# Performance work log

Hardware: AMD Instinct MI355X
Metric: run time of the kernel (lower is better)

## Reference

```python
import jax, jax.numpy as jnp
import numpy as np

SAMPLE_RATE = 44100
NUM_FILTERS = 3
FREQ_LO, FREQ_HI = 100.0, 3000.0
Q_LO, Q_HI = 1.0, 5.0
GAIN_LO, GAIN_HI = -24.0, 24.0


def _center_freqs():
    # power_ratio(i/N, f_lo, f_hi) = f_lo * (f_hi/f_lo)**(i/N)
    return [FREQ_LO * (FREQ_HI / FREQ_LO) ** (i / NUM_FILTERS) for i in range(NUM_FILTERS)]


def setup_inputs() -> dict:
    key = jax.random.key(0)
    k1, k2, k3 = jax.random.split(key, 3)
    audio = jax.random.normal(k1, (32, 441000), dtype=jnp.float32)  # [B, T]
    # Q sampled like power_ratio(u, q_lo, q_hi) = q_lo*(q_hi/q_lo)**u
    u = jax.random.uniform(k2, (NUM_FILTERS,), dtype=jnp.float32)
    qs = Q_LO * (Q_HI / Q_LO) ** u
    gains = jax.random.uniform(k3, (NUM_FILTERS,), dtype=jnp.float32,
                               minval=GAIN_LO, maxval=GAIN_HI)
    return {"audio": audio, "qs": qs, "gains": gains}


def _biquad(x, b0, b1, b2, a1, a2):
    """Direct-form-I biquad over time axis. x: [B, T]; coeffs normalized by a0."""
    B = x.shape[0]
    z = jnp.zeros((B,), x.dtype)

    def step(carry, xn):
        x1, x2, y1, y2 = carry
        yn = b0 * xn + b1 * x1 + b2 * x2 - a1 * y1 - a2 * y2
        return (xn, x1, yn, y1), yn

    _, y = jax.lax.scan(step, (z, z, z, z), x.T)  # scan over T
    return y.T


def _peaking_eq(audio, center_freq, gain, Q):
    # torchaudio.functional.equalizer_biquad coefficients
    w0 = 2.0 * jnp.pi * center_freq / SAMPLE_RATE
    alpha = jnp.sin(w0) / (2.0 * Q)
    A = jnp.exp(gain / 40.0 * jnp.log(10.0))  # 10**(gain/40)
    b0 = 1.0 + alpha * A
    b1 = -2.0 * jnp.cos(w0)
    b2 = 1.0 - alpha * A
    a0 = 1.0 + alpha / A
    a1 = -2.0 * jnp.cos(w0)
    a2 = 1.0 - alpha / A
    return _biquad(audio, b0 / a0, b1 / a0, b2 / a0, a1 / a0, a2 / a0)


def reference(audio, qs, gains):
    cfs = _center_freqs()
    for i in range(NUM_FILTERS):
        audio = _peaking_eq(audio, cfs[i], gains[i], qs[i])
    return audio
```

## Files before the change

kernel.cpp:

```cpp
#include <hip/hip_runtime.h>
#include <math.h>

#define SR      44100.0
#define T_LEN   441000
#define B_ROWS  32
#define CHUNK   32
#define NCH     13782
#define WPR     216
#define NWAVE   (B_ROWS * WPR)
#define NBLK    (NWAVE / 4)
#define NSEG    8
#define SEGCH   1724
#define ROUNDS  10

#define WS_T    0
#define WS_E    2048
#define WS_F    1576960

typedef __attribute__((address_space(1))) const void gconst_t;
typedef __attribute__((address_space(3))) void lds_t;
#define GL2LDS(gp, lp) __builtin_amdgcn_global_load_lds((gconst_t*)(gp), (lds_t*)(lp), 16, 0, 0)


#define COMPUTE_COEFS_TO_LDS(scoef, qs, gains) do { \
    if (threadIdx.x < 3) { \
      int f = threadIdx.x; \
      double cfq = 100.0 * exp(log(30.0) * (double)f / 3.0); \
      double w0 = 2.0 * M_PI * cfq / SR; \
      double alpha = sin(w0) / (2.0 * (double)qs[f]); \
      double Ag = exp((double)gains[f] * (2.302585092994045684 / 40.0)); \
      double a0 = 1.0 + alpha / Ag; \
      scoef[f*5+0] = (float)((1.0 + alpha * Ag) / a0); \
      scoef[f*5+1] = (float)((-2.0 * cos(w0)) / a0); \
      scoef[f*5+2] = (float)((1.0 - alpha * Ag) / a0); \
      scoef[f*5+3] = (float)((-2.0 * cos(w0)) / a0); \
      scoef[f*5+4] = (float)((1.0 - alpha / Ag) / a0); \
    } \
  } while (0)

#define LOAD_COEFS(cf) \
  const float b00=cf[0],b10=cf[1],b20=cf[2],a10=cf[3],a20=cf[4]; \
  const float b01=cf[5],b11=cf[6],b21=cf[7],a11=cf[8],a21=cf[9]; \
  const float b02=cf[10],b12=cf[11],b22=cf[12],a12=cf[13],a22=cf[14];

#define CASCADE_STEP(xx) do { \
    float y1 = fmaf(b00, (xx), s11); \
    s11 = fmaf(-a10, y1, fmaf(b10, (xx), s21)); \
    s21 = fmaf(-a20, y1, b20 * (xx)); \
    float y2 = fmaf(b01, y1, s12); \
    s12 = fmaf(-a11, y2, fmaf(b11, y1, s22)); \
    s22 = fmaf(-a21, y2, b21 * y1); \
    y3 = fmaf(b02, y2, s13); \
    s13 = fmaf(-a12, y3, fmaf(b12, y2, s23)); \
    s23 = fmaf(-a22, y3, b22 * y2); \
  } while (0)

#define MV6(dst, M, v, add) do { \
    _Pragma("unroll") \
    for (int _i = 0; _i < 6; _i++) { \
      float _s = (add)[_i]; \
      _Pragma("unroll") \
      for (int _k = 0; _k < 6; _k++) _s = fmaf((M)[_i*6+_k], (v)[_k], _s); \
      (dst)[_i] = _s; \
    } \
  } while (0)


__global__ __launch_bounds__(256) void kA_states(const float* __restrict__ x,
                                                 const float* __restrict__ qs,
                                                 const float* __restrict__ gains,
                                                 float* __restrict__ ws) {
  __shared__ float lds[4 * 2048];
  __shared__ float scoef[16];
  int wib = threadIdx.x >> 6, lane = threadIdx.x & 63;
  int gw = blockIdx.x * 4 + wib;
  int row = gw / WPR, wci = gw % WPR;
  long rowbase = (long)row * T_LEN;
  int s0 = wci << 11;
  int span4 = (min(2048, T_LEN - s0)) >> 2;
  const float4* xp = (const float4*)(x + rowbase + s0);
  float* slab = lds + (wib << 11);
  if (span4 == 512) {
    #pragma unroll
    for (int i = 0; i < 8; i++) {
      int s = (i << 6) + lane;
      int g = (s & ~7) | ((s & 7) ^ ((s >> 3) & 7));
      GL2LDS(xp + g, slab + (i << 8));
    }
  } else {
    #pragma unroll
    for (int i = 0; i < 8; i++) {
      int s = (i << 6) + lane;
      int g = (s & ~7) | ((s & 7) ^ ((s >> 3) & 7));
      if (g < span4) GL2LDS(xp + g, slab + (i << 8));
    }
  }
  COMPUTE_COEFS_TO_LDS(scoef, qs, gains);
  __syncthreads();
  int ci = (wci << 6) + lane;
  if (ci < NCH) {
    LOAD_COEFS(scoef);
    int rem = min(CHUNK, T_LEN - (ci << 5));
    int n4 = rem >> 2;
    const float* rowp = slab + (lane << 5);
    int xr = lane & 7;
    float s11=0,s21=0,s12=0,s22=0,s13=0,s23=0, y3;
    if (n4 == 8) {
      #pragma unroll
      for (int j4 = 0; j4 < 8; j4++) {
        float4 v = *(const float4*)(rowp + ((j4 ^ xr) << 2));
        CASCADE_STEP(v.x); CASCADE_STEP(v.y); CASCADE_STEP(v.z); CASCADE_STEP(v.w);
      }
    } else {
      for (int j4 = 0; j4 < n4; j4++) {
        float4 v = *(const float4*)(rowp + ((j4 ^ xr) << 2));
        CASCADE_STEP(v.x); CASCADE_STEP(v.y); CASCADE_STEP(v.z); CASCADE_STEP(v.w);
      }
    }
    (void)y3;
    float2* F = (float2*)(ws + WS_F + ((long)row * NCH + ci) * 6);
    F[0] = make_float2(s11, s21); F[1] = make_float2(s12, s22); F[2] = make_float2(s13, s23);
  }
}


__device__ __forceinline__ void mm6d(const double* X, const double* Y, double* Z, int t) {
  if (t < 36) {
    int i = t / 6, j = t % 6;
    double s = 0.0;
    #pragma unroll
    for (int k = 0; k < 6; k++) s += X[i*6+k] * Y[k*6+j];
    Z[t] = s;
  }
}

template<bool WANT_G>
__device__ __forceinline__ void scan_setup(const float* qs, const float* gains, int t,
                                           double* Da, double* Db, double* Dc, double* Dd,
                                           float* sW, float (*sV)[36], float* sG) {
  __shared__ double dco[3][5];
  if (t < 3) {
    int f = t;
    double cfq = 100.0 * exp(log(30.0) * (double)f / 3.0);
    double w0 = 2.0 * M_PI * cfq / SR;
    double alpha = sin(w0) / (2.0 * (double)qs[f]);
    double Ag = exp((double)gains[f] * (2.302585092994045684 / 40.0));
    double a0 = 1.0 + alpha / Ag;
    dco[f][0] = (1.0 + alpha * Ag) / a0;
    dco[f][1] = (-2.0 * cos(w0)) / a0;
    dco[f][2] = (1.0 - alpha * Ag) / a0;
    dco[f][3] = (-2.0 * cos(w0)) / a0;
    dco[f][4] = (1.0 - alpha / Ag) / a0;
  }
  __syncthreads();
  if (t == 0) {
    double u[7] = {0,0,0,0,0,0,1};
    for (int f = 0; f < 3; f++) {
      double b0=dco[f][0], b1=dco[f][1], b2=dco[f][2], a1=dco[f][3], a2=dco[f][4];
      double yv[7], s1p[7], s2p[7];
      for (int i = 0; i < 7; i++) {
        yv[i]  = b0 * u[i] + ((i == 2*f)   ? 1.0 : 0.0);
        s1p[i] = b1 * u[i] + ((i == 2*f+1) ? 1.0 : 0.0) - a1 * yv[i];
        s2p[i] = b2 * u[i] - a2 * yv[i];
      }
      for (int i = 0; i < 6; i++) { Da[(2*f)*6+i] = s1p[i]; Da[(2*f+1)*6+i] = s2p[i]; }
      for (int i = 0; i < 7; i++) u[i] = yv[i];
    }
  }
  if (WANT_G && t < 36) Dc[t] = (t % 7 == 0) ? 1.0 : 0.0;
  __syncthreads();
  mm6d(Da, Da, Db, t); __syncthreads();
  mm6d(Db, Db, Da, t); __syncthreads();
  mm6d(Da, Da, Db, t); __syncthreads();
  mm6d(Db, Db, Da, t); __syncthreads();
  mm6d(Da, Da, Db, t); __syncthreads();
  if (t < 36) sW[t] = (float)Db[t];
  mm6d(Db, Db, Da, t); __syncthreads();
  double* cur = Da; double* oth = Db;
  double* Gc = Dc; double* Gd = Dd;
  #pragma unroll
  for (int k = 0; k < ROUNDS; k++) {
    if (t < 36) sV[k][t] = (float)cur[t];
    if (WANT_G && ((SEGCH >> (k + 1)) & 1)) {
      __syncthreads();
      mm6d(Gc, cur, Gd, t); __syncthreads();
      double* tm = Gc; Gc = Gd; Gd = tm;
    }
    if (k < ROUNDS - 1) {
      __syncthreads();
      mm6d(cur, cur, oth, t); __syncthreads();
      double* tm = cur; cur = oth; oth = tm;
    }
  }
  if (WANT_G && t < 36) sG[t] = (float)Gc[t];
  __syncthreads();
}


__global__ __launch_bounds__(1024) void kB1_scan(const float* __restrict__ qs,
                                                 const float* __restrict__ gains,
                                                 float* __restrict__ ws) {
  int seg = blockIdx.x & 7, row = blockIdx.x >> 3, t = threadIdx.x;
  __shared__ double Da[36], Db[36], Dc[36], Dd[36];
  __shared__ float sW[36], sV[ROUNDS][36];
  __shared__ float bufA[1024][7], bufB[1024][7];
  scan_setup<false>(qs, gains, t, Da, Db, Dc, Dd, sW, sV, nullptr);

  int segstart = seg * SEGCH;
  int nch = min(SEGCH, NCH - segstart);
  int nact = nch >> 1;
  const float* F = ws + WS_F + ((long)row * NCH + segstart) * 6;
  float v[6] = {0,0,0,0,0,0};
  if (t < nact) {
    const float4* Fp = (const float4*)(F + 12 * t);
    float4 l0 = Fp[0], l1 = Fp[1], l2 = Fp[2];
    float f0[6] = {l0.x, l0.y, l0.z, l0.w, l1.x, l1.y};
    float f1[6] = {l1.z, l1.w, l2.x, l2.y, l2.z, l2.w};
    MV6(v, sW, f0, f1);
  }
  #pragma unroll
  for (int i = 0; i < 6; i++) bufA[t][i] = v[i];
  __syncthreads();
  float (*src)[7] = bufA, (*dst)[7] = bufB;
  for (int k = 0; k < ROUNDS; k++) {
    int d = 1 << k;
    float nv[6];
    if (t >= d) {
      MV6(nv, sV[k], src[t-d], src[t]);
    } else {
      #pragma unroll
      for (int i = 0; i < 6; i++) nv[i] = src[t][i];
    }
    #pragma unroll
    for (int i = 0; i < 6; i++) dst[t][i] = nv[i];
    __syncthreads();
    float (*tm)[7] = src; src = dst; dst = tm;
  }
  float* Ep = ws + WS_E + ((long)blockIdx.x * 1024 + t) * 6;
  if (t > 0) {
    #pragma unroll
    for (int i = 0; i < 6; i++) Ep[i] = src[t-1][i];
  } else {
    #pragma unroll
    for (int i = 0; i < 6; i++) Ep[i] = 0.0f;
  }
  if (t == nact - 1) {
    float* Tp = ws + WS_T + (long)blockIdx.x * 6;
    #pragma unroll
    for (int i = 0; i < 6; i++) Tp[i] = src[t][i];
  }
}


__global__ __launch_bounds__(1024) void kB2_inject(const float* __restrict__ qs,
                                                   const float* __restrict__ gains,
                                                   float* __restrict__ ws) {
  int seg = blockIdx.x & 7, row = blockIdx.x >> 3, t = threadIdx.x;
  __shared__ double Da[36], Db[36], Dc[36], Dd[36];
  __shared__ float sW[36], sV[ROUNDS][36], sG[36];
  __shared__ float sT[8][6], sO[6];
  scan_setup<true>(qs, gains, t, Da, Db, Dc, Dd, sW, sV, sG);
  if (t < 48) sT[t/6][t%6] = ws[WS_T + ((long)(row*8) + t/6) * 6 + t%6];
  __syncthreads();
  if (t == 0) {
    float o[6] = {0,0,0,0,0,0};
    for (int s2 = 0; s2 < seg; s2++) {
      float no[6];
      MV6(no, sG, o, sT[s2]);
      #pragma unroll
      for (int i = 0; i < 6; i++) o[i] = no[i];
    }
    #pragma unroll
    for (int i = 0; i < 6; i++) sO[i] = o[i];
  }
  __syncthreads();
  int segstart = seg * SEGCH;
  int nch = min(SEGCH, NCH - segstart);
  int nact = nch >> 1;
  if (t < nact) {
    float e[6];
    #pragma unroll
    for (int i = 0; i < 6; i++) e[i] = sO[i];
    for (int k = 0; k < ROUNDS; k++) {
      if ((t >> k) & 1) {
        float z[6] = {0,0,0,0,0,0}, ne[6];
        MV6(ne, sV[k], e, z);
        #pragma unroll
        for (int i = 0; i < 6; i++) e[i] = ne[i];
      }
    }
    const float* Er = ws + WS_E + ((long)blockIdx.x * 1024 + t) * 6;
    #pragma unroll
    for (int i = 0; i < 6; i++) e[i] += Er[i];
    float4* Fp = (float4*)(ws + WS_F + ((long)row * NCH + segstart) * 6 + 12 * t);
    float4 l0 = Fp[0], l1 = Fp[1], l2 = Fp[2];
    float f0[6] = {l0.x, l0.y, l0.z, l0.w, l1.x, l1.y};
    float e1[6];
    MV6(e1, sW, e, f0);
    (void)l2;
    Fp[0] = make_float4(e[0], e[1], e[2], e[3]);
    Fp[1] = make_float4(e[4], e[5], e1[0], e1[1]);
    Fp[2] = make_float4(e1[2], e1[3], e1[4], e1[5]);
  }
}


__global__ __launch_bounds__(256) void kC_emit(const float* __restrict__ x,
                                               const float* __restrict__ qs,
                                               const float* __restrict__ gains,
                                               float* __restrict__ y,
                                               const float* __restrict__ ws) {
  __shared__ float lds[4 * 2048];
  __shared__ float scoef[16];
  int wib = threadIdx.x >> 6, lane = threadIdx.x & 63;
  int gw = blockIdx.x * 4 + wib;
  int row = gw / WPR, wci = gw % WPR;
  long rowbase = (long)row * T_LEN;
  int s0 = wci << 11;
  int span4 = (min(2048, T_LEN - s0)) >> 2;
  const float4* xp = (const float4*)(x + rowbase + s0);
  float* slab = lds + (wib << 11);
  if (span4 == 512) {
    #pragma unroll
    for (int i = 0; i < 8; i++) {
      int s = (i << 6) + lane;
      int g = (s & ~7) | ((s & 7) ^ ((s >> 3) & 7));
      GL2LDS(xp + g, slab + (i << 8));
    }
  } else {
    #pragma unroll
    for (int i = 0; i < 8; i++) {
      int s = (i << 6) + lane;
      int g = (s & ~7) | ((s & 7) ^ ((s >> 3) & 7));
      if (g < span4) GL2LDS(xp + g, slab + (i << 8));
    }
  }
  COMPUTE_COEFS_TO_LDS(scoef, qs, gains);
  int ci = (wci << 6) + lane;
  float e0=0,e1=0,e2=0,e3=0,e4=0,e5=0;
  if (ci < NCH) {
    const float2* E = (const float2*)(ws + WS_F + ((long)row * NCH + ci) * 6);
    float2 a = E[0], b = E[1], c = E[2];
    e0=a.x; e1=a.y; e2=b.x; e3=b.y; e4=c.x; e5=c.y;
  }
  __syncthreads();
  if (ci < NCH) {
    LOAD_COEFS(scoef);
    float s11=e0, s21=e1, s12=e2, s22=e3, s13=e4, s23=e5;
    int rem = min(CHUNK, T_LEN - (ci << 5));
    int n4 = rem >> 2;
    float* rowp = slab + (lane << 5);
    int xr = lane & 7;
    float y3;
    if (n4 == 8) {
      #pragma unroll
      for (int j4 = 0; j4 < 8; j4++) {
        float* p = rowp + ((j4 ^ xr) << 2);
        float4 v = *(const float4*)p;
        float4 o;
        CASCADE_STEP(v.x); o.x = y3;
        CASCADE_STEP(v.y); o.y = y3;
        CASCADE_STEP(v.z); o.z = y3;
        CASCADE_STEP(v.w); o.w = y3;
        *(float4*)p = o;
      }
    } else {
      for (int j4 = 0; j4 < n4; j4++) {
        float* p = rowp + ((j4 ^ xr) << 2);
        float4 v = *(const float4*)p;
        float4 o;
        CASCADE_STEP(v.x); o.x = y3;
        CASCADE_STEP(v.y); o.y = y3;
        CASCADE_STEP(v.z); o.z = y3;
        CASCADE_STEP(v.w); o.w = y3;
        *(float4*)p = o;
      }
    }
  }
  __syncthreads();
  float4* yp = (float4*)(y + rowbase + s0);
  if (span4 == 512) {
    #pragma unroll
    for (int i = 0; i < 8; i++) {
      int g = (i << 6) + lane;
      int s = (g & ~7) | ((g & 7) ^ ((g >> 3) & 7));
      yp[g] = *(const float4*)(slab + (s << 2));
    }
  } else {
    #pragma unroll
    for (int i = 0; i < 8; i++) {
      int g = (i << 6) + lane;
      int s = (g & ~7) | ((g & 7) ^ ((g >> 3) & 7));
      if (g < span4) yp[g] = *(const float4*)(slab + (s << 2));
    }
  }
}

extern "C" void kernel_launch(void* const* d_in, const int* in_sizes, int n_in,
                              void* d_out, int out_size, void* d_ws, size_t ws_size,
                              hipStream_t stream) {
  const float* audio = (const float*)d_in[0];
  const float* qs    = (const float*)d_in[1];
  const float* gains = (const float*)d_in[2];
  float* out = (float*)d_out;
  float* ws  = (float*)d_ws;

  hipLaunchKernelGGL(kA_states, dim3(NBLK), dim3(256), 0, stream, audio, qs, gains, ws);
  hipLaunchKernelGGL(kB1_scan, dim3(B_ROWS * NSEG), dim3(1024), 0, stream, qs, gains, ws);
  hipLaunchKernelGGL(kB2_inject, dim3(B_ROWS * NSEG), dim3(1024), 0, stream, qs, gains, ws);
  hipLaunchKernelGGL(kC_emit, dim3(NBLK), dim3(256), 0, stream, audio, qs, gains, out, ws);
}
```

Before: 68.58 us.

## Fuse four-kernel biquad scan into one cooperative persistent kernel with grid syncs

Replaces the chain of four launches (chunk states, segment scan, inject, emit) with a single cooperative kernel. Each thread keeps its 32 input samples in registers across grid.sync barriers, so the input is read from global memory once, and the scan is re-partitioned into 32 segments per row run by the first 1024 blocks. It also adds readfirstlane for the filter coefficients. The aim is to remove launch gaps and the second input read, at the cost of grid-wide barriers, a serial per-block segment-prefix loop, and host-side occupancy queries on every call, with the old path kept as a fallback.

```diff
diff --git a/kernel.cpp b/kernel.cpp
--- a/kernel.cpp
+++ b/kernel.cpp
@@ -1,21 +1,29 @@
 #include <hip/hip_runtime.h>
+#include <hip/hip_cooperative_groups.h>
 #include <math.h>
+
+namespace cg = cooperative_groups;
 
 #define SR      44100.0
 #define T_LEN   441000
 #define B_ROWS  32
-#define CHUNK   32
 #define NCH     13782
+#define GCH     (B_ROWS * NCH)
+#define FNB     1723
+#define NSCAN   1024
+#define FSEGW   432
+#define FROUNDS 8
+
+#define FWS_T   0
+#define FWS_F   8192
+
+#define R5SEGCH 1724
+#define R5ROUNDS 10
+#define R5WS_T  0
+#define R5WS_E  2048
+#define R5WS_F  1576960
 #define WPR     216
-#define NWAVE   (B_ROWS * WPR)
-#define NBLK    (NWAVE / 4)
-#define NSEG    8
-#define SEGCH   1724
-#define ROUNDS  10
-
-#define WS_T    0
-#define WS_E    2048
-#define WS_F    1576960
+#define R5NBLK  1728
 
 typedef __attribute__((address_space(1))) const void gconst_t;
 typedef __attribute__((address_space(3))) void lds_t;
@@ -43,6 +51,14 @@
   const float b01=cf[5],b11=cf[6],b21=cf[7],a11=cf[8],a21=cf[9]; \
   const float b02=cf[10],b12=cf[11],b22=cf[12],a12=cf[13],a22=cf[14];
 
+__device__ __forceinline__ float rfl(float v) {
+  return __int_as_float(__builtin_amdgcn_readfirstlane(__float_as_int(v)));
+}
+#define LOAD_COEFS_RFL(cf) \
+  const float b00=rfl(cf[0]),b10=rfl(cf[1]),b20=rfl(cf[2]),a10=rfl(cf[3]),a20=rfl(cf[4]); \
+  const float b01=rfl(cf[5]),b11=rfl(cf[6]),b21=rfl(cf[7]),a11=rfl(cf[8]),a21=rfl(cf[9]); \
+  const float b02=rfl(cf[10]),b12=rfl(cf[11]),b22=rfl(cf[12]),a12=rfl(cf[13]),a22=rfl(cf[14]);
+
 #define CASCADE_STEP(xx) do { \
     float y1 = fmaf(b00, (xx), s11); \
     s11 = fmaf(-a10, y1, fmaf(b10, (xx), s21)); \
@@ -64,6 +80,322 @@
       (dst)[_i] = _s; \
     } \
   } while (0)
+
+__device__ __forceinline__ void mm6d(const double* X, const double* Y, double* Z, int t) {
+  if (t < 36) {
+    int i = t / 6, j = t % 6;
+    double s = 0.0;
+    #pragma unroll
+    for (int k = 0; k < 6; k++) s += X[i*6+k] * Y[k*6+j];
+    Z[t] = s;
+  }
+}
+
+
+#define STAGE_IN(h) do { \
+    _Pragma("unroll") \
+    for (int i = 0; i < 4; i++) { \
+      int t_ = (i << 6) + lane; \
+      int c_ = t_ >> 3; \
+      int q_ = (t_ & 7) ^ (c_ & 7); \
+      int gc_ = wc0 + ((h) << 5) + c_; \
+      unsigned r_ = (unsigned)gc_ / NCH; \
+      int ci_ = gc_ - (int)r_ * NCH; \
+      long s4_ = (long)r_ * 110250 + ci_ * 8 + q_; \
+      if (gc_ < GCH && s4_ < 3528000L) GL2LDS(xp4 + s4_, slab + (t_ << 2)); \
+    } \
+  } while (0)
+
+#define READ_HALF(h) do { \
+    if ((lane >> 5) == (h) && cvalid) { \
+      const float* rowp_ = slab + ((lane & 31) << 5); \
+      int xr_ = lane & 7; \
+      _Pragma("unroll") \
+      for (int j4 = 0; j4 < 8; j4++) a[j4] = *(const float4*)(rowp_ + ((j4 ^ xr_) << 2)); \
+    } \
+  } while (0)
+
+#define OUT_HALF(h) do { \
+    if ((lane >> 5) == (h) && cvalid) { \
+      float* rowp_ = slab + ((lane & 31) << 5); \
+      int xr_ = lane & 7; \
+      _Pragma("unroll") \
+      for (int j4 = 0; j4 < 8; j4++) *(float4*)(rowp_ + ((j4 ^ xr_) << 2)) = a[j4]; \
+    } \
+  } while (0)
+
+#define OUT_STORE(h) do { \
+    _Pragma("unroll") \
+    for (int i = 0; i < 4; i++) { \
+      int t_ = (i << 6) + lane; \
+      int c_ = t_ >> 3, q_ = t_ & 7; \
+      int gs_ = (t_ & ~7) | (q_ ^ (c_ & 7)); \
+      int gc_ = wc0 + ((h) << 5) + c_; \
+      unsigned r_ = (unsigned)gc_ / NCH; \
+      int ci_ = gc_ - (int)r_ * NCH; \
+      int n4c_ = (ci_ == NCH - 1) ? 2 : 8; \
+      if (gc_ < GCH && q_ < n4c_) \
+        ((float4*)y)[(long)r_ * 110250 + ci_ * 8 + q_] = *(const float4*)(slab + (gs_ << 2)); \
+    } \
+  } while (0)
+
+__global__ __launch_bounds__(256, 7) void fused(const float* __restrict__ x,
+                                                const float* __restrict__ qs,
+                                                const float* __restrict__ gains,
+                                                float* __restrict__ y,
+                                                float* __restrict__ ws) {
+  cg::grid_group grid = cg::this_grid();
+  __shared__ __align__(16) float smem[4736];
+  const int tid = threadIdx.x;
+  const int wib = tid >> 6, lane = tid & 63;
+  float* slab  = smem + (wib << 10);
+  float* scoef = smem + 4096;
+  float* sW    = smem + 4112;
+  float* sV    = smem + 4148;
+  float* sT    = smem + 4436;
+  float* sO    = smem + 4628;
+  float* sG    = smem + 4640;
+  const int wc0 = blockIdx.x * 256 + (wib << 6);
+  const int gchunk = blockIdx.x * 256 + tid;
+  const bool cvalid = gchunk < GCH;
+  const float4* xp4 = (const float4*)x;
+  float4 a[8];
+
+  STAGE_IN(0);
+  COMPUTE_COEFS_TO_LDS(scoef, qs, gains);
+  __syncthreads();
+  READ_HALF(0);
+  __syncthreads();
+  STAGE_IN(1);
+  __syncthreads();
+  READ_HALF(1);
+  LOAD_COEFS_RFL(scoef);
+  {
+    unsigned r = (unsigned)gchunk / NCH;
+    int ci = gchunk - (int)r * NCH;
+    int n4 = (ci == NCH - 1) ? 2 : 8;
+    if (cvalid) {
+      float s11=0,s21=0,s12=0,s22=0,s13=0,s23=0, y3;
+      if (n4 == 8) {
+        #pragma unroll
+        for (int j4 = 0; j4 < 8; j4++) {
+          CASCADE_STEP(a[j4].x); CASCADE_STEP(a[j4].y);
+          CASCADE_STEP(a[j4].z); CASCADE_STEP(a[j4].w);
+        }
+      } else {
+        CASCADE_STEP(a[0].x); CASCADE_STEP(a[0].y); CASCADE_STEP(a[0].z); CASCADE_STEP(a[0].w);
+        CASCADE_STEP(a[1].x); CASCADE_STEP(a[1].y); CASCADE_STEP(a[1].z); CASCADE_STEP(a[1].w);
+      }
+      (void)y3;
+      float2* F2 = (float2*)(ws + FWS_F + (long)gchunk * 6);
+      F2[0] = make_float2(s11, s21); F2[1] = make_float2(s12, s22); F2[2] = make_float2(s13, s23);
+    }
+  }
+  grid.sync();
+
+  const bool isScan = blockIdx.x < NSCAN;
+  if (isScan) {
+    double* D = (double*)smem;
+    double* Da = D, *Db = D+36, *Dc = D+72, *Dd = D+108, *dco = D+144;
+    if (tid < 3) {
+      int f = tid;
+      double cfq = 100.0 * exp(log(30.0) * (double)f / 3.0);
+      double w0 = 2.0 * M_PI * cfq / SR;
+      double alpha = sin(w0) / (2.0 * (double)qs[f]);
+      double Ag = exp((double)gains[f] * (2.302585092994045684 / 40.0));
+      double a0 = 1.0 + alpha / Ag;
+      dco[f*5+0] = (1.0 + alpha * Ag) / a0;
+      dco[f*5+1] = (-2.0 * cos(w0)) / a0;
+      dco[f*5+2] = (1.0 - alpha * Ag) / a0;
+      dco[f*5+3] = (-2.0 * cos(w0)) / a0;
+      dco[f*5+4] = (1.0 - alpha / Ag) / a0;
+    }
+    __syncthreads();
+    if (tid == 0) {
+      double u[7] = {0,0,0,0,0,0,1};
+      for (int f = 0; f < 3; f++) {
+        double b0=dco[f*5+0], b1=dco[f*5+1], b2=dco[f*5+2], a1=dco[f*5+3], a2=dco[f*5+4];
+        double yv[7], s1p[7], s2p[7];
+        for (int i = 0; i < 7; i++) {
+          yv[i]  = b0 * u[i] + ((i == 2*f)   ? 1.0 : 0.0);
+          s1p[i] = b1 * u[i] + ((i == 2*f+1) ? 1.0 : 0.0) - a1 * yv[i];
+          s2p[i] = b2 * u[i] - a2 * yv[i];
+        }
+        for (int i = 0; i < 6; i++) { Da[(2*f)*6+i] = s1p[i]; Da[(2*f+1)*6+i] = s2p[i]; }
+        for (int i = 0; i < 7; i++) u[i] = yv[i];
+      }
+    }
+    __syncthreads();
+    mm6d(Da, Da, Db, tid); __syncthreads();
+    mm6d(Db, Db, Da, tid); __syncthreads();
+    mm6d(Da, Da, Db, tid); __syncthreads();
+    mm6d(Db, Db, Da, tid); __syncthreads();
+    mm6d(Da, Da, Db, tid); __syncthreads();
+    if (tid < 36) { sW[tid] = (float)Db[tid]; Dc[tid] = (tid % 7 == 0) ? 1.0 : 0.0; }
+    __syncthreads();
+    mm6d(Db, Db, Da, tid); __syncthreads();
+    {
+      double* cur = Da; double* oth = Db; double* Gc = Dc; double* Gd = Dd;
+      #pragma unroll
+      for (int k = 0; k < FROUNDS; k++) {
+        if (tid < 36) sV[k*36 + tid] = (float)cur[tid];
+        if ((FSEGW >> (k + 1)) & 1) {
+          __syncthreads();
+          mm6d(Gc, cur, Gd, tid); __syncthreads();
+          double* tm = Gc; Gc = Gd; Gd = tm;
+        }
+        if (k < FROUNDS - 1) {
+          __syncthreads();
+          mm6d(cur, cur, oth, tid); __syncthreads();
+          double* tm = cur; cur = oth; oth = tm;
+        }
+      }
+      if (tid < 36) sG[tid] = (float)Gc[tid];
+    }
+    __syncthreads();
+
+    int srow = blockIdx.x >> 5, seg = blockIdx.x & 31;
+    int segstart = seg * FSEGW;
+    int nact = (seg == 31) ? 195 : 216;
+    float* bufA = smem;
+    float* bufB = smem + 1792;
+    float e_rel[6], f0[6];
+    {
+      float v[6] = {0,0,0,0,0,0};
+      if (tid < nact) {
+        const float4* Fp = (const float4*)(ws + FWS_F + ((long)srow*NCH + segstart + 2*tid) * 6);
+        float4 l0 = Fp[0], l1 = Fp[1], l2 = Fp[2];
+        f0[0]=l0.x; f0[1]=l0.y; f0[2]=l0.z; f0[3]=l0.w; f0[4]=l1.x; f0[5]=l1.y;
+        float f1[6] = {l1.z, l1.w, l2.x, l2.y, l2.z, l2.w};
+        MV6(v, sW, f0, f1);
+      }
+      #pragma unroll
+      for (int i = 0; i < 6; i++) bufA[tid*7 + i] = v[i];
+      __syncthreads();
+      float* src = bufA; float* dst = bufB;
+      for (int k = 0; k < FROUNDS; k++) {
+        int d = 1 << k;
+        float nv[6];
+        if (tid >= d) { MV6(nv, sV + k*36, src + (tid-d)*7, src + tid*7); }
+        else { 
+          #pragma unroll
+          for (int i = 0; i < 6; i++) nv[i] = src[tid*7 + i];
+        }
+        #pragma unroll
+        for (int i = 0; i < 6; i++) dst[tid*7 + i] = nv[i];
+        __syncthreads();
+        float* tm = src; src = dst; dst = tm;
+      }
+      if (tid > 0) {
+        #pragma unroll
+        for (int i = 0; i < 6; i++) e_rel[i] = src[(tid-1)*7 + i];
+      } else {
+        #pragma unroll
+        for (int i = 0; i < 6; i++) e_rel[i] = 0.0f;
+      }
+      if (tid == nact - 1) {
+        #pragma unroll
+        for (int i = 0; i < 6; i++) ws[FWS_T + (long)blockIdx.x * 6 + i] = src[tid*7 + i];
+      }
+    }
+    grid.sync();
+    if (tid < 192) sT[tid] = ws[FWS_T + srow*192 + tid];
+    __syncthreads();
+    if (tid == 0) {
+      float o[6] = {0,0,0,0,0,0};
+      for (int s2 = 0; s2 < seg; s2++) {
+        float no[6];
+        MV6(no, sG, o, sT + s2*6);
+        #pragma unroll
+        for (int i = 0; i < 6; i++) o[i] = no[i];
+      }
+      #pragma unroll
+      for (int i = 0; i < 6; i++) sO[i] = o[i];
+    }
+    __syncthreads();
+    if (tid < nact) {
+      float e[6];
+      #pragma unroll
+      for (int i = 0; i < 6; i++) e[i] = sO[i];
+      float z6[6] = {0,0,0,0,0,0};
+      for (int k = 0; k < FROUNDS; k++) {
+        if ((tid >> k) & 1) {
+          float ne[6];
+          MV6(ne, sV + k*36, e, z6);
+          #pragma unroll
+          for (int i = 0; i < 6; i++) e[i] = ne[i];
+        }
+      }
+      #pragma unroll
+      for (int i = 0; i < 6; i++) e[i] += e_rel[i];
+      float e1[6];
+      MV6(e1, sW, e, f0);
+      float4* Fp = (float4*)(ws + FWS_F + ((long)srow*NCH + segstart + 2*tid) * 6);
+      Fp[0] = make_float4(e[0], e[1], e[2], e[3]);
+      Fp[1] = make_float4(e[4], e[5], e1[0], e1[1]);
+      Fp[2] = make_float4(e1[2], e1[3], e1[4], e1[5]);
+    }
+    grid.sync();
+    STAGE_IN(0);
+    __syncthreads();
+    READ_HALF(0);
+    __syncthreads();
+    STAGE_IN(1);
+    __syncthreads();
+    READ_HALF(1);
+  } else {
+    grid.sync();
+    grid.sync();
+  }
+
+  {
+    float e0=0,e1v=0,e2=0,e3=0,e4=0,e5=0;
+    if (cvalid) {
+      const float2* E = (const float2*)(ws + FWS_F + (long)gchunk * 6);
+      float2 p0 = E[0], p1 = E[1], p2 = E[2];
+      e0=p0.x; e1v=p0.y; e2=p1.x; e3=p1.y; e4=p2.x; e5=p2.y;
+    }
+    unsigned r = (unsigned)gchunk / NCH;
+    int ci = gchunk - (int)r * NCH;
+    int n4 = (ci == NCH - 1) ? 2 : 8;
+    if (cvalid) {
+      float s11=e0, s21=e1v, s12=e2, s22=e3, s13=e4, s23=e5;
+      float y3;
+      if (n4 == 8) {
+        #pragma unroll
+        for (int j4 = 0; j4 < 8; j4++) {
+          float4 v = a[j4], o;
+          CASCADE_STEP(v.x); o.x = y3;
+          CASCADE_STEP(v.y); o.y = y3;
+          CASCADE_STEP(v.z); o.z = y3;
+          CASCADE_STEP(v.w); o.w = y3;
+          a[j4] = o;
+        }
+      } else {
+        float4 v = a[0], o;
+        CASCADE_STEP(v.x); o.x = y3;
+        CASCADE_STEP(v.y); o.y = y3;
+        CASCADE_STEP(v.z); o.z = y3;
+        CASCADE_STEP(v.w); o.w = y3;
+        a[0] = o;
+        v = a[1];
+        CASCADE_STEP(v.x); o.x = y3;
+        CASCADE_STEP(v.y); o.y = y3;
+        CASCADE_STEP(v.z); o.z = y3;
+        CASCADE_STEP(v.w); o.w = y3;
+        a[1] = o;
+      }
+    }
+  }
+  __syncthreads();
+  OUT_HALF(0);
+  __syncthreads();
+  OUT_STORE(0);
+  __syncthreads();
+  OUT_HALF(1);
+  __syncthreads();
+  OUT_STORE(1);
+}
 
 
 __global__ __launch_bounds__(256) void kA_states(const float* __restrict__ x,
@@ -80,57 +412,29 @@
   int span4 = (min(2048, T_LEN - s0)) >> 2;
   const float4* xp = (const float4*)(x + rowbase + s0);
   float* slab = lds + (wib << 11);
-  if (span4 == 512) {
-    #pragma unroll
-    for (int i = 0; i < 8; i++) {
-      int s = (i << 6) + lane;
-      int g = (s & ~7) | ((s & 7) ^ ((s >> 3) & 7));
-      GL2LDS(xp + g, slab + (i << 8));
-    }
-  } else {
-    #pragma unroll
-    for (int i = 0; i < 8; i++) {
-      int s = (i << 6) + lane;
-      int g = (s & ~7) | ((s & 7) ^ ((s >> 3) & 7));
-      if (g < span4) GL2LDS(xp + g, slab + (i << 8));
-    }
+  #pragma unroll
+  for (int i = 0; i < 8; i++) {
+    int s = (i << 6) + lane;
+    int g = (s & ~7) | ((s & 7) ^ ((s >> 3) & 7));
+    if (g < span4) GL2LDS(xp + g, slab + (i << 8));
   }
   COMPUTE_COEFS_TO_LDS(scoef, qs, gains);
   __syncthreads();
   int ci = (wci << 6) + lane;
   if (ci < NCH) {
     LOAD_COEFS(scoef);
-    int rem = min(CHUNK, T_LEN - (ci << 5));
+    int rem = min(32, T_LEN - (ci << 5));
     int n4 = rem >> 2;
     const float* rowp = slab + (lane << 5);
     int xr = lane & 7;
     float s11=0,s21=0,s12=0,s22=0,s13=0,s23=0, y3;
-    if (n4 == 8) {
-      #pragma unroll
-      for (int j4 = 0; j4 < 8; j4++) {
-        float4 v = *(const float4*)(rowp + ((j4 ^ xr) << 2));
-        CASCADE_STEP(v.x); CASCADE_STEP(v.y); CASCADE_STEP(v.z); CASCADE_STEP(v.w);
-      }
-    } else {
-      for (int j4 = 0; j4 < n4; j4++) {
-        float4 v = *(const float4*)(rowp + ((j4 ^ xr) << 2));
-        CASCADE_STEP(v.x); CASCADE_STEP(v.y); CASCADE_STEP(v.z); CASCADE_STEP(v.w);
-      }
+    for (int j4 = 0; j4 < n4; j4++) {
+      float4 v = *(const float4*)(rowp + ((j4 ^ xr) << 2));
+      CASCADE_STEP(v.x); CASCADE_STEP(v.y); CASCADE_STEP(v.z); CASCADE_STEP(v.w);
     }
     (void)y3;
-    float2* F = (float2*)(ws + WS_F + ((long)row * NCH + ci) * 6);
+    float2* F = (float2*)(ws + R5WS_F + ((long)row * NCH + ci) * 6);
     F[0] = make_float2(s11, s21); F[1] = make_float2(s12, s22); F[2] = make_float2(s13, s23);
-  }
-}
-
-
-__device__ __forceinline__ void mm6d(const double* X, const double* Y, double* Z, int t) {
-  if (t < 36) {
-    int i = t / 6, j = t % 6;
-    double s = 0.0;
-    #pragma unroll
-    for (int k = 0; k < 6; k++) s += X[i*6+k] * Y[k*6+j];
-    Z[t] = s;
   }
 }
 
@@ -179,14 +483,14 @@
   double* cur = Da; double* oth = Db;
   double* Gc = Dc; double* Gd = Dd;
   #pragma unroll
-  for (int k = 0; k < ROUNDS; k++) {
+  for (int k = 0; k < R5ROUNDS; k++) {
     if (t < 36) sV[k][t] = (float)cur[t];
-    if (WANT_G && ((SEGCH >> (k + 1)) & 1)) {
+    if (WANT_G && ((R5SEGCH >> (k + 1)) & 1)) {
       __syncthreads();
       mm6d(Gc, cur, Gd, t); __syncthreads();
       double* tm = Gc; Gc = Gd; Gd = tm;
     }
-    if (k < ROUNDS - 1) {
+    if (k < R5ROUNDS - 1) {
       __syncthreads();
       mm6d(cur, cur, oth, t); __syncthreads();
       double* tm = cur; cur = oth; oth = tm;
@@ -195,21 +499,19 @@
   if (WANT_G && t < 36) sG[t] = (float)Gc[t];
   __syncthreads();
 }
-
 
 __global__ __launch_bounds__(1024) void kB1_scan(const float* __restrict__ qs,
                                                  const float* __restrict__ gains,
                                                  float* __restrict__ ws) {
   int seg = blockIdx.x & 7, row = blockIdx.x >> 3, t = threadIdx.x;
   __shared__ double Da[36], Db[36], Dc[36], Dd[36];
-  __shared__ float sW[36], sV[ROUNDS][36];
+  __shared__ float sW[36], sV[R5ROUNDS][36];
   __shared__ float bufA[1024][7], bufB[1024][7];
   scan_setup<false>(qs, gains, t, Da, Db, Dc, Dd, sW, sV, nullptr);
-
-  int segstart = seg * SEGCH;
-  int nch = min(SEGCH, NCH - segstart);
+  int segstart = seg * R5SEGCH;
+  int nch = min(R5SEGCH, NCH - segstart);
   int nact = nch >> 1;
-  const float* F = ws + WS_F + ((long)row * NCH + segstart) * 6;
+  const float* F = ws + R5WS_F + ((long)row * NCH + segstart) * 6;
   float v[6] = {0,0,0,0,0,0};
   if (t < nact) {
     const float4* Fp = (const float4*)(F + 12 * t);
@@ -222,12 +524,11 @@
   for (int i = 0; i < 6; i++) bufA[t][i] = v[i];
   __syncthreads();
   float (*src)[7] = bufA, (*dst)[7] = bufB;
-  for (int k = 0; k < ROUNDS; k++) {
+  for (int k = 0; k < R5ROUNDS; k++) {
     int d = 1 << k;
     float nv[6];
-    if (t >= d) {
-      MV6(nv, sV[k], src[t-d], src[t]);
-    } else {
+    if (t >= d) { MV6(nv, sV[k], src[t-d], src[t]); }
+    else {
       #pragma unroll
       for (int i = 0; i < 6; i++) nv[i] = src[t][i];
     }
@@ -236,7 +537,7 @@
     __syncthreads();
     float (*tm)[7] = src; src = dst; dst = tm;
   }
-  float* Ep = ws + WS_E + ((long)blockIdx.x * 1024 + t) * 6;
+  float* Ep = ws + R5WS_E + ((long)blockIdx.x * 1024 + t) * 6;
   if (t > 0) {
     #pragma unroll
     for (int i = 0; i < 6; i++) Ep[i] = src[t-1][i];
@@ -245,22 +546,21 @@
     for (int i = 0; i < 6; i++) Ep[i] = 0.0f;
   }
   if (t == nact - 1) {
-    float* Tp = ws + WS_T + (long)blockIdx.x * 6;
+    float* Tp = ws + R5WS_T + (long)blockIdx.x * 6;
     #pragma unroll
     for (int i = 0; i < 6; i++) Tp[i] = src[t][i];
   }
 }
-
 
 __global__ __launch_bounds__(1024) void kB2_inject(const float* __restrict__ qs,
                                                    const float* __restrict__ gains,
                                                    float* __restrict__ ws) {
   int seg = blockIdx.x & 7, row = blockIdx.x >> 3, t = threadIdx.x;
   __shared__ double Da[36], Db[36], Dc[36], Dd[36];
-  __shared__ float sW[36], sV[ROUNDS][36], sG[36];
+  __shared__ float sW[36], sV[R5ROUNDS][36], sG[36];
   __shared__ float sT[8][6], sO[6];
   scan_setup<true>(qs, gains, t, Da, Db, Dc, Dd, sW, sV, sG);
-  if (t < 48) sT[t/6][t%6] = ws[WS_T + ((long)(row*8) + t/6) * 6 + t%6];
+  if (t < 48) sT[t/6][t%6] = ws[R5WS_T + ((long)(row*8) + t/6) * 6 + t%6];
   __syncthreads();
   if (t == 0) {
     float o[6] = {0,0,0,0,0,0};
@@ -274,14 +574,14 @@
     for (int i = 0; i < 6; i++) sO[i] = o[i];
   }
   __syncthreads();
-  int segstart = seg * SEGCH;
-  int nch = min(SEGCH, NCH - segstart);
+  int segstart = seg * R5SEGCH;
+  int nch = min(R5SEGCH, NCH - segstart);
   int nact = nch >> 1;
   if (t < nact) {
     float e[6];
     #pragma unroll
     for (int i = 0; i < 6; i++) e[i] = sO[i];
-    for (int k = 0; k < ROUNDS; k++) {
+    for (int k = 0; k < R5ROUNDS; k++) {
       if ((t >> k) & 1) {
         float z[6] = {0,0,0,0,0,0}, ne[6];
         MV6(ne, sV[k], e, z);
@@ -289,21 +589,19 @@
         for (int i = 0; i < 6; i++) e[i] = ne[i];
       }
     }
-    const float* Er = ws + WS_E + ((long)blockIdx.x * 1024 + t) * 6;
+    const float* Er = ws + R5WS_E + ((long)blockIdx.x * 1024 + t) * 6;
     #pragma unroll
     for (int i = 0; i < 6; i++) e[i] += Er[i];
-    float4* Fp = (float4*)(ws + WS_F + ((long)row * NCH + segstart) * 6 + 12 * t);
-    float4 l0 = Fp[0], l1 = Fp[1], l2 = Fp[2];
+    float4* Fp = (float4*)(ws + R5WS_F + ((long)row * NCH + segstart) * 6 + 12 * t);
+    float4 l0 = Fp[0], l1 = Fp[1];
     float f0[6] = {l0.x, l0.y, l0.z, l0.w, l1.x, l1.y};
     float e1[6];
     MV6(e1, sW, e, f0);
-    (void)l2;
     Fp[0] = make_float4(e[0], e[1], e[2], e[3]);
     Fp[1] = make_float4(e[4], e[5], e1[0], e1[1]);
     Fp[2] = make_float4(e1[2], e1[3], e1[4], e1[5]);
   }
 }
-
 
 __global__ __launch_bounds__(256) void kC_emit(const float* __restrict__ x,
                                                const float* __restrict__ qs,
@@ -320,79 +618,47 @@
   int span4 = (min(2048, T_LEN - s0)) >> 2;
   const float4* xp = (const float4*)(x + rowbase + s0);
   float* slab = lds + (wib << 11);
-  if (span4 == 512) {
-    #pragma unroll
-    for (int i = 0; i < 8; i++) {
-      int s = (i << 6) + lane;
-      int g = (s & ~7) | ((s & 7) ^ ((s >> 3) & 7));
-      GL2LDS(xp + g, slab + (i << 8));
-    }
-  } else {
-    #pragma unroll
-    for (int i = 0; i < 8; i++) {
-      int s = (i << 6) + lane;
-      int g = (s & ~7) | ((s & 7) ^ ((s >> 3) & 7));
-      if (g < span4) GL2LDS(xp + g, slab + (i << 8));
-    }
+  #pragma unroll
+  for (int i = 0; i < 8; i++) {
+    int s = (i << 6) + lane;
+    int g = (s & ~7) | ((s & 7) ^ ((s >> 3) & 7));
+    if (g < span4) GL2LDS(xp + g, slab + (i << 8));
   }
   COMPUTE_COEFS_TO_LDS(scoef, qs, gains);
   int ci = (wci << 6) + lane;
   float e0=0,e1=0,e2=0,e3=0,e4=0,e5=0;
   if (ci < NCH) {
-    const float2* E = (const float2*)(ws + WS_F + ((long)row * NCH + ci) * 6);
-    float2 a = E[0], b = E[1], c = E[2];
-    e0=a.x; e1=a.y; e2=b.x; e3=b.y; e4=c.x; e5=c.y;
+    const float2* E = (const float2*)(ws + R5WS_F + ((long)row * NCH + ci) * 6);
+    float2 p0 = E[0], p1 = E[1], p2 = E[2];
+    e0=p0.x; e1=p0.y; e2=p1.x; e3=p1.y; e4=p2.x; e5=p2.y;
   }
   __syncthreads();
   if (ci < NCH) {
     LOAD_COEFS(scoef);
     float s11=e0, s21=e1, s12=e2, s22=e3, s13=e4, s23=e5;
-    int rem = min(CHUNK, T_LEN - (ci << 5));
+    int rem = min(32, T_LEN - (ci << 5));
     int n4 = rem >> 2;
     float* rowp = slab + (lane << 5);
     int xr = lane & 7;
     float y3;
-    if (n4 == 8) {
-      #pragma unroll
-      for (int j4 = 0; j4 < 8; j4++) {
-        float* p = rowp + ((j4 ^ xr) << 2);
-        float4 v = *(const float4*)p;
-        float4 o;
-        CASCADE_STEP(v.x); o.x = y3;
-        CASCADE_STEP(v.y); o.y = y3;
-        CASCADE_STEP(v.z); o.z = y3;
-        CASCADE_STEP(v.w); o.w = y3;
-        *(float4*)p = o;
-      }
-    } else {
-      for (int j4 = 0; j4 < n4; j4++) {
-        float* p = rowp + ((j4 ^ xr) << 2);
-        float4 v = *(const float4*)p;
-        float4 o;
-        CASCADE_STEP(v.x); o.x = y3;
-        CASCADE_STEP(v.y); o.y = y3;
-        CASCADE_STEP(v.z); o.z = y3;
-        CASCADE_STEP(v.w); o.w = y3;
-        *(float4*)p = o;
-      }
+    for (int j4 = 0; j4 < n4; j4++) {
+      float* p = rowp + ((j4 ^ xr) << 2);
+      float4 v = *(const float4*)p;
+      float4 o;
+      CASCADE_STEP(v.x); o.x = y3;
+      CASCADE_STEP(v.y); o.y = y3;
+      CASCADE_STEP(v.z); o.z = y3;
+      CASCADE_STEP(v.w); o.w = y3;
+      *(float4*)p = o;
     }
   }
   __syncthreads();
   float4* yp = (float4*)(y + rowbase + s0);
-  if (span4 == 512) {
-    #pragma unroll
-    for (int i = 0; i < 8; i++) {
-      int g = (i << 6) + lane;
-      int s = (g & ~7) | ((g & 7) ^ ((g >> 3) & 7));
-      yp[g] = *(const float4*)(slab + (s << 2));
-    }
-  } else {
-    #pragma unroll
-    for (int i = 0; i < 8; i++) {
-      int g = (i << 6) + lane;
-      int s = (g & ~7) | ((g & 7) ^ ((g >> 3) & 7));
-      if (g < span4) yp[g] = *(const float4*)(slab + (s << 2));
-    }
+  #pragma unroll
+  for (int i = 0; i < 8; i++) {
+    int g = (i << 6) + lane;
+    int s = (g & ~7) | ((g & 7) ^ ((g >> 3) & 7));
+    if (g < span4) yp[g] = *(const float4*)(lds + (wib << 11) + (s << 2));
   }
 }
 
@@ -405,8 +671,24 @@
   float* out = (float*)d_out;
   float* ws  = (float*)d_ws;
 
-  hipLaunchKernelGGL(kA_states, dim3(NBLK), dim3(256), 0, stream, audio, qs, gains, ws);
-  hipLaunchKernelGGL(kB1_scan, dim3(B_ROWS * NSEG), dim3(1024), 0, stream, qs, gains, ws);
-  hipLaunchKernelGGL(kB2_inject, dim3(B_ROWS * NSEG), dim3(1024), 0, stream, qs, gains, ws);
-  hipLaunchKernelGGL(kC_emit, dim3(NBLK), dim3(256), 0, stream, audio, qs, gains, out, ws);
-}
+  int dev = 0;
+  (void)hipGetDevice(&dev);
+  int nb = 0;
+  (void)hipOccupancyMaxActiveBlocksPerMultiprocessor(&nb, fused, 256, 0);
+  int ncu = 0;
+  (void)hipDeviceGetAttribute(&ncu, hipDeviceAttributeMultiprocessorCount, dev);
+
+  hipError_t st = hipErrorUnknown;
+  if ((long)nb * ncu >= FNB) {
+    void* kargs[] = {(void*)&audio, (void*)&qs, (void*)&gains, (void*)&out, (void*)&ws};
+    st = hipLaunchCooperativeKernel((const void*)fused, dim3(FNB), dim3(256),
+                                    kargs, 0, stream);
+  }
+  if (st != hipSuccess) {
+    (void)hipGetLastError();
+    hipLaunchKernelGGL(kA_states, dim3(R5NBLK), dim3(256), 0, stream, audio, qs, gains, ws);
+    hipLaunchKernelGGL(kB1_scan, dim3(B_ROWS * 8), dim3(1024), 0, stream, qs, gains, ws);
+    hipLaunchKernelGGL(kB2_inject, dim3(B_ROWS * 8), dim3(1024), 0, stream, qs, gains, ws);
+    hipLaunchKernelGGL(kC_emit, dim3(R5NBLK), dim3(256), 0, stream, audio, qs, gains, out, ws);
+  }
+}
```

Measured after the change: 69.67 us. Within noise of the previous version (+1.6%).

## Merge scan and inject kernels, move cross-segment carry injection into emit kernel

Applied to the files above, without the earlier changes.

Removes the separate kB2_inject kernel. The scan kernel now writes each segment's local exclusive prefix state directly into the F buffer, plus the segment totals and the power matrices to workspace. The emit kernel then computes the per-segment carry with the G matrix and propagates it to each chunk using binary powers of the transition matrix before running the cascade. This saves one kernel launch and the extra workspace round trip for E, at the cost of up to 11 6x6 matrix-vector products per thread plus a serial carry loop in emit. It also relies on block 0 writing the matrices that every block in the later kernel reads, which is safe because the writes happen in a previous launch on the same stream.

```diff
diff --git a/kernel.cpp b/kernel.cpp
--- a/kernel.cpp
+++ b/kernel.cpp
@@ -4,8 +4,8 @@
 #define SR      44100.0
 #define T_LEN   441000
 #define B_ROWS  32
-#define CHUNK   32
 #define NCH     13782
+#define GCH     (B_ROWS * NCH)
 #define WPR     216
 #define NWAVE   (B_ROWS * WPR)
 #define NBLK    (NWAVE / 4)
@@ -13,9 +13,9 @@
 #define SEGCH   1724
 #define ROUNDS  10
 
-#define WS_T    0
-#define WS_E    2048
-#define WS_F    1576960
+#define WS_MAT  0
+#define WS_T    512
+#define WS_F    4096
 
 typedef __attribute__((address_space(1))) const void gconst_t;
 typedef __attribute__((address_space(3))) void lds_t;
@@ -65,6 +65,16 @@
     } \
   } while (0)
 
+__device__ __forceinline__ void mm6d(const double* X, const double* Y, double* Z, int t) {
+  if (t < 36) {
+    int i = t / 6, j = t % 6;
+    double s = 0.0;
+    #pragma unroll
+    for (int k = 0; k < 6; k++) s += X[i*6+k] * Y[k*6+j];
+    Z[t] = s;
+  }
+}
+
 
 __global__ __launch_bounds__(256) void kA_states(const float* __restrict__ x,
                                                  const float* __restrict__ qs,
@@ -100,7 +110,7 @@
   int ci = (wci << 6) + lane;
   if (ci < NCH) {
     LOAD_COEFS(scoef);
-    int rem = min(CHUNK, T_LEN - (ci << 5));
+    int rem = min(32, T_LEN - (ci << 5));
     int n4 = rem >> 2;
     const float* rowp = slab + (lane << 5);
     int xr = lane & 7;
@@ -124,17 +134,6 @@
 }
 
 
-__device__ __forceinline__ void mm6d(const double* X, const double* Y, double* Z, int t) {
-  if (t < 36) {
-    int i = t / 6, j = t % 6;
-    double s = 0.0;
-    #pragma unroll
-    for (int k = 0; k < 6; k++) s += X[i*6+k] * Y[k*6+j];
-    Z[t] = s;
-  }
-}
-
-template<bool WANT_G>
 __device__ __forceinline__ void scan_setup(const float* qs, const float* gains, int t,
                                            double* Da, double* Db, double* Dc, double* Dd,
                                            float* sW, float (*sV)[36], float* sG) {
@@ -167,7 +166,7 @@
       for (int i = 0; i < 7; i++) u[i] = yv[i];
     }
   }
-  if (WANT_G && t < 36) Dc[t] = (t % 7 == 0) ? 1.0 : 0.0;
+  if (t < 36) Dc[t] = (t % 7 == 0) ? 1.0 : 0.0;
   __syncthreads();
   mm6d(Da, Da, Db, t); __syncthreads();
   mm6d(Db, Db, Da, t); __syncthreads();
@@ -181,7 +180,7 @@
   #pragma unroll
   for (int k = 0; k < ROUNDS; k++) {
     if (t < 36) sV[k][t] = (float)cur[t];
-    if (WANT_G && ((SEGCH >> (k + 1)) & 1)) {
+    if ((SEGCH >> (k + 1)) & 1) {
       __syncthreads();
       mm6d(Gc, cur, Gd, t); __syncthreads();
       double* tm = Gc; Gc = Gd; Gd = tm;
@@ -192,29 +191,35 @@
       double* tm = cur; cur = oth; oth = tm;
     }
   }
-  if (WANT_G && t < 36) sG[t] = (float)Gc[t];
-  __syncthreads();
-}
-
-
-__global__ __launch_bounds__(1024) void kB1_scan(const float* __restrict__ qs,
-                                                 const float* __restrict__ gains,
-                                                 float* __restrict__ ws) {
+  if (t < 36) sG[t] = (float)Gc[t];
+  __syncthreads();
+}
+
+
+__global__ __launch_bounds__(1024) void kB_scan(const float* __restrict__ qs,
+                                                const float* __restrict__ gains,
+                                                float* __restrict__ ws) {
   int seg = blockIdx.x & 7, row = blockIdx.x >> 3, t = threadIdx.x;
   __shared__ double Da[36], Db[36], Dc[36], Dd[36];
-  __shared__ float sW[36], sV[ROUNDS][36];
+  __shared__ float sW[36], sV[ROUNDS][36], sG[36];
   __shared__ float bufA[1024][7], bufB[1024][7];
-  scan_setup<false>(qs, gains, t, Da, Db, Dc, Dd, sW, sV, nullptr);
-
+  scan_setup(qs, gains, t, Da, Db, Dc, Dd, sW, sV, sG);
+  if (blockIdx.x == 0 && t < 36) {
+    ws[WS_MAT + t] = sW[t];
+    #pragma unroll
+    for (int k = 0; k < ROUNDS; k++) ws[WS_MAT + (k + 1) * 36 + t] = sV[k][t];
+    ws[WS_MAT + 11 * 36 + t] = sG[t];
+  }
   int segstart = seg * SEGCH;
   int nch = min(SEGCH, NCH - segstart);
   int nact = nch >> 1;
-  const float* F = ws + WS_F + ((long)row * NCH + segstart) * 6;
+  float* F = ws + WS_F + ((long)row * NCH + segstart) * 6;
   float v[6] = {0,0,0,0,0,0};
+  float f0[6] = {0,0,0,0,0,0};
   if (t < nact) {
     const float4* Fp = (const float4*)(F + 12 * t);
     float4 l0 = Fp[0], l1 = Fp[1], l2 = Fp[2];
-    float f0[6] = {l0.x, l0.y, l0.z, l0.w, l1.x, l1.y};
+    f0[0]=l0.x; f0[1]=l0.y; f0[2]=l0.z; f0[3]=l0.w; f0[4]=l1.x; f0[5]=l1.y;
     float f1[6] = {l1.z, l1.w, l2.x, l2.y, l2.z, l2.w};
     MV6(v, sW, f0, f1);
   }
@@ -225,9 +230,8 @@
   for (int k = 0; k < ROUNDS; k++) {
     int d = 1 << k;
     float nv[6];
-    if (t >= d) {
-      MV6(nv, sV[k], src[t-d], src[t]);
-    } else {
+    if (t >= d) { MV6(nv, sV[k], src[t-d], src[t]); }
+    else {
       #pragma unroll
       for (int i = 0; i < 6; i++) nv[i] = src[t][i];
     }
@@ -236,68 +240,23 @@
     __syncthreads();
     float (*tm)[7] = src; src = dst; dst = tm;
   }
-  float* Ep = ws + WS_E + ((long)blockIdx.x * 1024 + t) * 6;
-  if (t > 0) {
-    #pragma unroll
-    for (int i = 0; i < 6; i++) Ep[i] = src[t-1][i];
-  } else {
-    #pragma unroll
-    for (int i = 0; i < 6; i++) Ep[i] = 0.0f;
-  }
   if (t == nact - 1) {
     float* Tp = ws + WS_T + (long)blockIdx.x * 6;
     #pragma unroll
     for (int i = 0; i < 6; i++) Tp[i] = src[t][i];
   }
-}
-
-
-__global__ __launch_bounds__(1024) void kB2_inject(const float* __restrict__ qs,
-                                                   const float* __restrict__ gains,
-                                                   float* __restrict__ ws) {
-  int seg = blockIdx.x & 7, row = blockIdx.x >> 3, t = threadIdx.x;
-  __shared__ double Da[36], Db[36], Dc[36], Dd[36];
-  __shared__ float sW[36], sV[ROUNDS][36], sG[36];
-  __shared__ float sT[8][6], sO[6];
-  scan_setup<true>(qs, gains, t, Da, Db, Dc, Dd, sW, sV, sG);
-  if (t < 48) sT[t/6][t%6] = ws[WS_T + ((long)(row*8) + t/6) * 6 + t%6];
-  __syncthreads();
-  if (t == 0) {
-    float o[6] = {0,0,0,0,0,0};
-    for (int s2 = 0; s2 < seg; s2++) {
-      float no[6];
-      MV6(no, sG, o, sT[s2]);
-      #pragma unroll
-      for (int i = 0; i < 6; i++) o[i] = no[i];
-    }
-    #pragma unroll
-    for (int i = 0; i < 6; i++) sO[i] = o[i];
-  }
-  __syncthreads();
-  int segstart = seg * SEGCH;
-  int nch = min(SEGCH, NCH - segstart);
-  int nact = nch >> 1;
   if (t < nact) {
     float e[6];
-    #pragma unroll
-    for (int i = 0; i < 6; i++) e[i] = sO[i];
-    for (int k = 0; k < ROUNDS; k++) {
-      if ((t >> k) & 1) {
-        float z[6] = {0,0,0,0,0,0}, ne[6];
-        MV6(ne, sV[k], e, z);
-        #pragma unroll
-        for (int i = 0; i < 6; i++) e[i] = ne[i];
-      }
-    }
-    const float* Er = ws + WS_E + ((long)blockIdx.x * 1024 + t) * 6;
-    #pragma unroll
-    for (int i = 0; i < 6; i++) e[i] += Er[i];
-    float4* Fp = (float4*)(ws + WS_F + ((long)row * NCH + segstart) * 6 + 12 * t);
-    float4 l0 = Fp[0], l1 = Fp[1], l2 = Fp[2];
-    float f0[6] = {l0.x, l0.y, l0.z, l0.w, l1.x, l1.y};
+    if (t > 0) {
+      #pragma unroll
+      for (int i = 0; i < 6; i++) e[i] = src[t-1][i];
+    } else {
+      #pragma unroll
+      for (int i = 0; i < 6; i++) e[i] = 0.0f;
+    }
     float e1[6];
     MV6(e1, sW, e, f0);
-    (void)l2;
+    float4* Fp = (float4*)(F + 12 * t);
     Fp[0] = make_float4(e[0], e[1], e[2], e[3]);
     Fp[1] = make_float4(e[4], e[5], e1[0], e1[1]);
     Fp[2] = make_float4(e1[2], e1[3], e1[4], e1[5]);
@@ -312,9 +271,14 @@
                                                const float* __restrict__ ws) {
   __shared__ float lds[4 * 2048];
   __shared__ float scoef[16];
-  int wib = threadIdx.x >> 6, lane = threadIdx.x & 63;
+  __shared__ float smat[432];
+  __shared__ float sTT[96];
+  __shared__ float sO[96];
+  int tid = threadIdx.x;
+  int wib = tid >> 6, lane = tid & 63;
   int gw = blockIdx.x * 4 + wib;
   int row = gw / WPR, wci = gw % WPR;
+  int rowA = (blockIdx.x * 4) / WPR;
   long rowbase = (long)row * T_LEN;
   int s0 = wci << 11;
   int span4 = (min(2048, T_LEN - s0)) >> 2;
@@ -335,19 +299,59 @@
       if (g < span4) GL2LDS(xp + g, slab + (i << 8));
     }
   }
+  for (int i = tid; i < 432; i += 256) smat[i] = ws[WS_MAT + i];
+  {
+    int rowB = (blockIdx.x * 4 + 3) / WPR;
+    if (tid < 96) {
+      int r = (tid < 48) ? rowA : rowB;
+      int j = tid - ((tid < 48) ? 0 : 48);
+      sTT[tid] = ws[WS_T + (long)r * 48 + j];
+    }
+  }
   COMPUTE_COEFS_TO_LDS(scoef, qs, gains);
   int ci = (wci << 6) + lane;
-  float e0=0,e1=0,e2=0,e3=0,e4=0,e5=0;
+  float e0=0,e1v=0,e2=0,e3=0,e4=0,e5=0;
   if (ci < NCH) {
     const float2* E = (const float2*)(ws + WS_F + ((long)row * NCH + ci) * 6);
-    float2 a = E[0], b = E[1], c = E[2];
-    e0=a.x; e1=a.y; e2=b.x; e3=b.y; e4=c.x; e5=c.y;
+    float2 p0 = E[0], p1 = E[1], p2 = E[2];
+    e0=p0.x; e1v=p0.y; e2=p1.x; e3=p1.y; e4=p2.x; e5=p2.y;
+  }
+  __syncthreads();
+  if (tid < 16) {
+    int rsel = tid >> 3, sg = tid & 7;
+    const float* Gm = smat + 11 * 36;
+    float o[6] = {0,0,0,0,0,0};
+    for (int s2 = 0; s2 < sg; s2++) {
+      float no[6];
+      MV6(no, Gm, o, &sTT[rsel * 48 + s2 * 6]);
+      #pragma unroll
+      for (int i = 0; i < 6; i++) o[i] = no[i];
+    }
+    #pragma unroll
+    for (int i = 0; i < 6; i++) sO[tid * 6 + i] = o[i];
   }
   __syncthreads();
   if (ci < NCH) {
     LOAD_COEFS(scoef);
-    float s11=e0, s21=e1, s12=e2, s22=e3, s13=e4, s23=e5;
-    int rem = min(CHUNK, T_LEN - (ci << 5));
+    int seg = ci / SEGCH;
+    int d = ci - seg * SEGCH;
+    int rsel = (row == rowA) ? 0 : 1;
+    const float* op = sO + (rsel * 8 + seg) * 6;
+    float m[6];
+    #pragma unroll
+    for (int i = 0; i < 6; i++) m[i] = op[i];
+    float z6[6] = {0,0,0,0,0,0};
+    #pragma unroll
+    for (int k = 0; k < 11; k++) {
+      if ((d >> k) & 1) {
+        float nm[6];
+        MV6(nm, smat + k * 36, m, z6);
+        #pragma unroll
+        for (int i = 0; i < 6; i++) m[i] = nm[i];
+      }
+    }
+    float s11=e0+m[0], s21=e1v+m[1], s12=e2+m[2], s22=e3+m[3], s13=e4+m[4], s23=e5+m[5];
+    int rem = min(32, T_LEN - (ci << 5));
     int n4 = rem >> 2;
     float* rowp = slab + (lane << 5);
     int xr = lane & 7;
@@ -406,7 +410,6 @@
   float* ws  = (float*)d_ws;
 
   hipLaunchKernelGGL(kA_states, dim3(NBLK), dim3(256), 0, stream, audio, qs, gains, ws);
-  hipLaunchKernelGGL(kB1_scan, dim3(B_ROWS * NSEG), dim3(1024), 0, stream, qs, gains, ws);
-  hipLaunchKernelGGL(kB2_inject, dim3(B_ROWS * NSEG), dim3(1024), 0, stream, qs, gains, ws);
+  hipLaunchKernelGGL(kB_scan, dim3(B_ROWS * NSEG), dim3(1024), 0, stream, qs, gains, ws);
   hipLaunchKernelGGL(kC_emit, dim3(NBLK), dim3(256), 0, stream, audio, qs, gains, out, ws);
 }
```

After: 68.08 us. No clear change (-0.7%).
